# Kernel optimization log

Hardware: AMD Instinct MI355X
Metric: run time of the kernel (lower is better)

The kernel has to match this reference:

```python
import jax, jax.numpy as jnp
import numpy as np

GROUPS = 4
KLD_SCALE = 10.0
COMMIT_COST = 0.25


def setup_inputs() -> dict:
    key = jax.random.key(0)
    k1, k2, k3, k4 = jax.random.split(key, 4)
    B, H, C = 8, 4096, 512
    n_embed, d = 512, C // GROUPS
    return {
        "z": jax.random.normal(k1, (B, H, C), dtype=jnp.float32),
        "embed_w": jax.random.normal(k2, (n_embed, d), dtype=jnp.float32),
        "proj_w": jax.random.normal(k3, (C, C), dtype=jnp.float32) * (1.0 / np.sqrt(C)),
        "proj_b": jax.random.normal(k4, (C,), dtype=jnp.float32) * 0.01,
    }


def reference(z, embed_w, proj_w, proj_b):
    B, H, C = z.shape
    d = C // GROUPS
    sg = jax.lax.stop_gradient
    # split channels into groups -> [B, H*groups, d]
    z_e = z.reshape(B, H * GROUPS, d)
    flat = z_e.reshape(-1, d)  # [N, d]
    dist = ((flat ** 2).sum(1, keepdims=True)
            - 2.0 * flat @ embed_w.T
            + (embed_w ** 2).sum(1)[None, :])  # [N, n_embed]
    ind = jnp.argmin(dist, axis=1).reshape(B, H * GROUPS)  # (-dist).max == dist.min
    z_q = embed_w[ind]  # [B, H*groups, d]
    diff = KLD_SCALE * (COMMIT_COST * jnp.mean((sg(z_q) - z_e) ** 2)
                        + jnp.mean((z_q - sg(z_e)) ** 2))
    # straight-through estimator
    z_q = z_e + sg(z_q - z_e)
    z_q = z_q.reshape(B, H, C)
    out = z_q @ proj_w.T + proj_b
    return out, diff, ind
```

## Files before the change

kernel.cpp:

```cpp
#include <hip/hip_runtime.h>

constexpr int D         = 128;
constexpr int NE        = 512;
constexpr int NROWS     = 131072;
constexpr int CC        = 512;
constexpr int OUT_ELEMS = 16777216;


using half8  = __attribute__((ext_vector_type(8))) _Float16;
using f32x16 = __attribute__((ext_vector_type(16))) float;

#define F16_MINNORM 6.103515625e-05f

__global__ void eprep_kernel(const float* __restrict__ embed,
                             unsigned short* __restrict__ esw,
                             float* __restrict__ entab,
                             float* __restrict__ ws_diff) {
    const int chunk = blockIdx.x;
    const int tid = threadIdx.x;
    const int cl = tid >> 3;
    const int seg = tid & 7;
    const float* src = embed + (size_t)(chunk * 32 + cl) * D + seg * 16;
    unsigned short* cb = esw + (size_t)chunk * 8192;

    float ss = 0.f;
#pragma unroll
    for (int g2 = 0; g2 < 2; g2++) {
        float4 a = ((const float4*)src)[g2 * 2 + 0];
        float4 b = ((const float4*)src)[g2 * 2 + 1];
        float v[8] = {a.x, a.y, a.z, a.w, b.x, b.y, b.z, b.w};
        half8 t1, t2;
#pragma unroll
        for (int i = 0; i < 8; i++) {
            ss += v[i] * v[i];
            float m2 = -2.0f * v[i];
            float m2c = (__builtin_fabsf(m2) < F16_MINNORM) ? 0.0f : m2;
            _Float16 h = (_Float16)m2c;
            float r = m2 - (float)h;
            t1[i] = h;
            t2[i] = (_Float16)(r * 2048.0f);
        }
        const int idx = seg * 512 + g2 * 256 + cl * 8;
        *(half8*)(cb + idx) = t1;
        *(half8*)(cb + 4096 + idx) = t2;
    }
    ss += __shfl_down(ss, 4, 8);
    ss += __shfl_down(ss, 2, 8);
    ss += __shfl_down(ss, 1, 8);
    if (seg == 0) entab[chunk * 32 + cl] = ss;
    if (chunk == 0 && tid == 0) ws_diff[0] = 0.0f;
}

#define AS_STRIDE 68
#define AS_S4 17

__launch_bounds__(256, 4)
__global__ void pgemm_kernel(const float* __restrict__ embed,
                             const float* __restrict__ projw,
                             float* __restrict__ P) {
    __shared__ float As[64 * AS_STRIDE];
    __shared__ float Bs[64 * AS_STRIDE];
    const int tid = threadIdx.x;
    const int cbase = blockIdx.x * 64;
    const int jbase = blockIdx.y * 64;
    const int g = blockIdx.z;
    const int tx = tid & 15, ty = tid >> 4;
    const int r = tid >> 2, seg = tid & 3;

    float acc[4][4];
#pragma unroll
    for (int i = 0; i < 4; i++)
#pragma unroll
        for (int j = 0; j < 4; j++) acc[i][j] = 0.f;

    for (int kb = 0; kb < D; kb += 64) {
        const float4* asrc = (const float4*)(embed + (size_t)(jbase + r) * D + kb + seg * 16);
        const float4* bsrc = (const float4*)(projw + (size_t)(cbase + r) * CC + g * D + kb + seg * 16);
        float4* adst = (float4*)&As[r * AS_STRIDE + seg * 16];
        float4* bdst = (float4*)&Bs[r * AS_STRIDE + seg * 16];
#pragma unroll
        for (int q = 0; q < 4; q++) { adst[q] = asrc[q]; bdst[q] = bsrc[q]; }
        __syncthreads();

        const float4* as4 = (const float4*)As;
        const float4* bs4 = (const float4*)Bs;
#pragma unroll 4
        for (int kk = 0; kk < 16; kk++) {
            float4 a[4], b[4];
#pragma unroll
            for (int i = 0; i < 4; i++) a[i] = as4[(ty + 16 * i) * AS_S4 + kk];
#pragma unroll
            for (int j = 0; j < 4; j++) b[j] = bs4[(tx + 16 * j) * AS_S4 + kk];
#pragma unroll
            for (int i = 0; i < 4; i++)
#pragma unroll
                for (int j = 0; j < 4; j++)
                    acc[i][j] += a[i].x * b[j].x + a[i].y * b[j].y +
                                 a[i].z * b[j].z + a[i].w * b[j].w;
        }
        __syncthreads();
    }
#pragma unroll
    for (int j = 0; j < 4; j++) {
#pragma unroll
        for (int i = 0; i < 4; i++)
            P[(size_t)g * 262144 + (size_t)(jbase + ty + 16 * i) * CC + cbase + tx + 16 * j] =
                acc[i][j];
    }
}

__global__ __launch_bounds__(256, 3)
void argmin_fused_kernel(const float* __restrict__ z,
                         const unsigned short* __restrict__ esw,
                         const float* __restrict__ entab,
                         const float* __restrict__ P,
                         const float* __restrict__ projb,
                         float* __restrict__ ws_diff,
                         float* __restrict__ ind_f,
                         float* __restrict__ out) {
    __shared__ unsigned char ebuf[32768];
    __shared__ int ind_s[128];
    const int tid = threadIdx.x;
    const int lane = tid & 63;
    const int wave = tid >> 6;
    const int h5 = lane >> 5, l5 = lane & 31;
    const int rb = blockIdx.x * 128 + wave * 32;

    half8 x1[8], x2[8];
    float xn = 0.f;
    {
        const float* zr = z + (size_t)(rb + l5) * D + h5 * 8;
#pragma unroll
        for (int kk = 0; kk < 8; kk++) {
            float4 a = *(const float4*)(zr + kk * 16);
            float4 b = *(const float4*)(zr + kk * 16 + 4);
            float v[8] = {a.x, a.y, a.z, a.w, b.x, b.y, b.z, b.w};
            half8 t1, t2;
#pragma unroll
            for (int i = 0; i < 8; i++) {
                xn += v[i] * v[i];
                float vc = (__builtin_fabsf(v[i]) < F16_MINNORM) ? 0.0f : v[i];
                _Float16 h = (_Float16)vc;
                float r = v[i] - (float)h;
                t1[i] = h;
                t2[i] = (_Float16)(r * 2048.0f);
            }
            x1[kk] = t1; x2[kk] = t2;
        }
    }

    float minv = 3.0e38f;
    int   mini = 0;

    auto stage = [&](int c, int b) {
        const unsigned char* s = (const unsigned char*)esw + (size_t)c * 16384 +
                                 wave * 4096 + lane * 16;
        unsigned char* d = &ebuf[b * 16384 + wave * 4096];
#pragma unroll
        for (int it = 0; it < 4; it++)
            __builtin_amdgcn_global_load_lds(
                (const __attribute__((address_space(1))) unsigned int*)(s + it * 1024),
                (__attribute__((address_space(3))) unsigned int*)(d + it * 1024),
                16, 0, 0);
    };

    stage(0, 0);
    __syncthreads();

#pragma unroll 1
    for (int c = 0; c < 16; c++) {
        if (c < 15) stage(c + 1, (c + 1) & 1);
        const unsigned char* ldsb = &ebuf[(c & 1) * 16384];

        float4 enr[4];
#pragma unroll
        for (int u = 0; u < 4; u++)
            enr[u] = *(const float4*)(entab + c * 32 + h5 * 4 + u * 8);

        f32x16 accA = (f32x16)(0.0f), accB = (f32x16)(0.0f);
#pragma unroll
        for (int kk = 0; kk < 8; kk++) {
            const int fo = kk * 1024 + h5 * 512 + l5 * 16;
            half8 e1 = *(const half8*)(ldsb + fo);
            half8 e2 = *(const half8*)(ldsb + 8192 + fo);
            accA = __builtin_amdgcn_mfma_f32_32x32x16_f16(e1, x1[kk], accA, 0, 0, 0);
            accB = __builtin_amdgcn_mfma_f32_32x32x16_f16(e1, x2[kk], accB, 0, 0, 0);
            accB = __builtin_amdgcn_mfma_f32_32x32x16_f16(e2, x1[kk], accB, 0, 0, 0);
        }

        const int cb2 = c * 32 + h5 * 4;
#pragma unroll
        for (int r = 0; r < 16; r++) {
            const float en = ((const float*)&enr[r >> 2])[r & 3];
            const int cand = cb2 + (r & 3) + 8 * (r >> 2);
            float d0 = fmaf(accB[r], 4.8828125e-4f, accA[r]) + en;
            if (d0 < minv) { minv = d0; mini = cand; }
        }
        __syncthreads();
    }

    {
        float ov = __shfl_xor(minv, 32);
        int oi = __shfl_xor(mini, 32);
        if (ov < minv || (ov == minv && oi < mini)) { minv = ov; mini = oi; }
    }
    if (lane < 32) {
        ind_f[rb + l5] = (float)mini;
        ind_s[wave * 32 + l5] = mini;
    }

    float xfull = xn + __shfl_xor(xn, 32);
    float v = (lane < 32) ? (xfull + minv) : 0.0f;
#pragma unroll
    for (int off = 32; off; off >>= 1) v += __shfl_down(v, off);
    if (lane == 0) atomicAdd(ws_diff, v);

    __syncthreads();

    const int mb = blockIdx.x * 32;
    const int c4 = tid & 127;
    const int mh = (tid >> 7) * 16;
    const float4 bias = ((const float4*)projb)[c4];
    const float4* P4 = (const float4*)P;
#pragma unroll 4
    for (int u = 0; u < 16; u++) {
        const int ml = mh + u;
        float4 acc = bias;
#pragma unroll
        for (int g = 0; g < 4; g++) {
            const int ig = ind_s[ml * 4 + g];
            float4 p = P4[(size_t)g * 65536 + (size_t)ig * 128 + c4];
            acc.x += p.x; acc.y += p.y; acc.z += p.z; acc.w += p.w;
        }
        ((float4*)out)[(size_t)(mb + ml) * 128 + c4] = acc;
    }
}

__global__ void finalize_kernel(const float* __restrict__ ws_diff,
                                float* __restrict__ diff_out) {
    diff_out[0] = 12.5f * ws_diff[0] * (1.0f / 16777216.0f);
}

extern "C" void kernel_launch(void* const* d_in, const int* in_sizes, int n_in,
                              void* d_out, int out_size, void* d_ws, size_t ws_size,
                              hipStream_t stream) {
    const float* z     = (const float*)d_in[0];
    const float* embed = (const float*)d_in[1];
    const float* projw = (const float*)d_in[2];
    const float* projb = (const float*)d_in[3];

    float* out      = (float*)d_out;
    float* diff_out = out + OUT_ELEMS;
    float* ind_f    = out + OUT_ELEMS + 1;

    char* wsb = (char*)d_ws;
    float* ws_diff = (float*)wsb;
    float* entab = (float*)(wsb + 1024);
    unsigned short* esw = (unsigned short*)(wsb + 4096);
    float* P = (float*)(wsb + 266240);

    eprep_kernel<<<16, 256, 0, stream>>>(embed, esw, entab, ws_diff);
    pgemm_kernel<<<dim3(8, 8, 4), 256, 0, stream>>>(embed, projw, P);
    argmin_fused_kernel<<<NROWS / 128, 256, 0, stream>>>(z, esw, entab, P, projb,
                                                         ws_diff, ind_f, out);
    finalize_kernel<<<1, 1, 0, stream>>>(ws_diff, diff_out);
}
```

Before: 218.9 us.

## Fold code norms into MFMA accumulator init via bf16 split ones-product

```diff
diff --git a/kernel.cpp b/kernel.cpp
--- a/kernel.cpp
+++ b/kernel.cpp
@@ -8,20 +8,30 @@
 
 
 using half8  = __attribute__((ext_vector_type(8))) _Float16;
+using short8 = __attribute__((ext_vector_type(8))) short;
 using f32x16 = __attribute__((ext_vector_type(16))) float;
 
 #define F16_MINNORM 6.103515625e-05f
+
+static __device__ __forceinline__ unsigned short bf16rn(float x) {
+    union { float f; unsigned u; } c; c.f = x;
+    unsigned u = c.u;
+    return (unsigned short)((u + 0x7FFFu + ((u >> 16) & 1u)) >> 16);
+}
+static __device__ __forceinline__ float bf16tof(unsigned short h) {
+    union { unsigned u; float f; } c; c.u = ((unsigned)h) << 16;
+    return c.f;
+}
 
 __global__ void eprep_kernel(const float* __restrict__ embed,
                              unsigned short* __restrict__ esw,
-                             float* __restrict__ entab,
                              float* __restrict__ ws_diff) {
     const int chunk = blockIdx.x;
     const int tid = threadIdx.x;
     const int cl = tid >> 3;
     const int seg = tid & 7;
     const float* src = embed + (size_t)(chunk * 32 + cl) * D + seg * 16;
-    unsigned short* cb = esw + (size_t)chunk * 8192;
+    unsigned short* cb = esw + (size_t)chunk * 8704;
 
     float ss = 0.f;
 #pragma unroll
@@ -47,7 +57,18 @@
     ss += __shfl_down(ss, 4, 8);
     ss += __shfl_down(ss, 2, 8);
     ss += __shfl_down(ss, 1, 8);
-    if (seg == 0) entab[chunk * 32 + cl] = ss;
+    if (seg == 0) {
+        unsigned short e0 = bf16rn(ss);
+        float r1 = ss - bf16tof(e0);
+        unsigned short e1 = bf16rn(r1);
+        unsigned short e2 = bf16rn(r1 - bf16tof(e1));
+        short8 en = (short8)0;
+        en[0] = (short)e0; en[1] = (short)e1; en[2] = (short)e2;
+        *(short8*)(cb + 8192 + cl * 8) = en;
+    }
+    if (seg == 1) {
+        *(short8*)(cb + 8192 + 256 + cl * 8) = (short8)0;
+    }
     if (chunk == 0 && tid == 0) ws_diff[0] = 0.0f;
 }
 
@@ -109,20 +130,19 @@
     }
 }
 
-__global__ __launch_bounds__(256, 3)
+__global__ __launch_bounds__(256, 2)
 void argmin_fused_kernel(const float* __restrict__ z,
                          const unsigned short* __restrict__ esw,
-                         const float* __restrict__ entab,
                          const float* __restrict__ P,
                          const float* __restrict__ projb,
                          float* __restrict__ ws_diff,
                          float* __restrict__ ind_f,
                          float* __restrict__ out) {
-    __shared__ unsigned char ebuf[32768];
+    __shared__ unsigned char ebuf[34816];
     __shared__ int ind_s[128];
     const int tid = threadIdx.x;
     const int lane = tid & 63;
-    const int wave = tid >> 6;
+    const int wave = __builtin_amdgcn_readfirstlane(tid >> 6);
     const int h5 = lane >> 5, l5 = lane & 31;
     const int rb = blockIdx.x * 128 + wave * 32;
 
@@ -148,19 +168,19 @@
             x1[kk] = t1; x2[kk] = t2;
         }
     }
+    short8 ones = (short8)0;
+    if (h5 == 0) { ones[0] = (short)0x3F80; ones[1] = (short)0x3F80; ones[2] = (short)0x3F80; }
 
     float minv = 3.0e38f;
     int   mini = 0;
 
     auto stage = [&](int c, int b) {
-        const unsigned char* s = (const unsigned char*)esw + (size_t)c * 16384 +
-                                 wave * 4096 + lane * 16;
-        unsigned char* d = &ebuf[b * 16384 + wave * 4096];
-#pragma unroll
-        for (int it = 0; it < 4; it++)
+        const unsigned char* s = (const unsigned char*)esw + (size_t)c * 17408 + lane * 16;
+        unsigned char* d = &ebuf[b * 17408] + lane * 16;
+        for (int seg = wave; seg < 17; seg += 4)
             __builtin_amdgcn_global_load_lds(
-                (const __attribute__((address_space(1))) unsigned int*)(s + it * 1024),
-                (__attribute__((address_space(3))) unsigned int*)(d + it * 1024),
+                (const __attribute__((address_space(1))) unsigned int*)(s + seg * 1024),
+                (__attribute__((address_space(3))) unsigned int*)(d + seg * 1024),
                 16, 0, 0);
     };
 
@@ -170,14 +190,14 @@
 #pragma unroll 1
     for (int c = 0; c < 16; c++) {
         if (c < 15) stage(c + 1, (c + 1) & 1);
-        const unsigned char* ldsb = &ebuf[(c & 1) * 16384];
-
-        float4 enr[4];
-#pragma unroll
-        for (int u = 0; u < 4; u++)
-            enr[u] = *(const float4*)(entab + c * 32 + h5 * 4 + u * 8);
-
-        f32x16 accA = (f32x16)(0.0f), accB = (f32x16)(0.0f);
+        const unsigned char* ldsb = &ebuf[(c & 1) * 17408];
+
+        f32x16 accA, accB;
+        {
+            short8 aen = *(const short8*)(ldsb + 16384 + h5 * 512 + l5 * 16);
+            accA = __builtin_amdgcn_mfma_f32_32x32x16_bf16(aen, ones, (f32x16)(0.0f), 0, 0, 0);
+        }
+        accB = (f32x16)(0.0f);
 #pragma unroll
         for (int kk = 0; kk < 8; kk++) {
             const int fo = kk * 1024 + h5 * 512 + l5 * 16;
@@ -191,9 +211,8 @@
         const int cb2 = c * 32 + h5 * 4;
 #pragma unroll
         for (int r = 0; r < 16; r++) {
-            const float en = ((const float*)&enr[r >> 2])[r & 3];
             const int cand = cb2 + (r & 3) + 8 * (r >> 2);
-            float d0 = fmaf(accB[r], 4.8828125e-4f, accA[r]) + en;
+            float d0 = fmaf(accB[r], 4.8828125e-4f, accA[r]);
             if (d0 < minv) { minv = d0; mini = cand; }
         }
         __syncthreads();
@@ -255,13 +274,12 @@
 
     char* wsb = (char*)d_ws;
     float* ws_diff = (float*)wsb;
-    float* entab = (float*)(wsb + 1024);
-    unsigned short* esw = (unsigned short*)(wsb + 4096);
-    float* P = (float*)(wsb + 266240);
-
-    eprep_kernel<<<16, 256, 0, stream>>>(embed, esw, entab, ws_diff);
+    unsigned short* esw = (unsigned short*)(wsb + 1024);
+    float* P = (float*)(wsb + 280576);
+
+    eprep_kernel<<<16, 256, 0, stream>>>(embed, esw, ws_diff);
     pgemm_kernel<<<dim3(8, 8, 4), 256, 0, stream>>>(embed, projw, P);
-    argmin_fused_kernel<<<NROWS / 128, 256, 0, stream>>>(z, esw, entab, P, projb,
+    argmin_fused_kernel<<<NROWS / 128, 256, 0, stream>>>(z, esw, P, projb,
                                                          ws_diff, ind_f, out);
     finalize_kernel<<<1, 1, 0, stream>>>(ws_diff, diff_out);
 }
```

After: 223.9 us. 1.02x slower.
